# Optimization experiments

Measured on AMD Instinct MI355X. Metric: run time of the kernel, lower is better.

## Reference

```python
import jax, jax.numpy as jnp
import numpy as np

F0_DIM, PH_DIM, MIDI_DIM, DUR_DIM = 64, 128, 64, 64
COND = 256
TOTAL = F0_DIM + PH_DIM + MIDI_DIM + DUR_DIM  # 320
EPS = 1e-5


def setup_inputs() -> dict:
    key = jax.random.key(0)
    ks = jax.random.split(key, 16)
    B, T = 16, 4096
    inp = {
        "f0": jax.random.uniform(ks[0], (B, T), jnp.float32) * 400.0 + 80.0,
        "phone": jax.random.randint(ks[1], (B, T), 0, 100, jnp.int32),
        "duration": jax.random.uniform(ks[2], (B, T), jnp.float32),
        "midi": jax.random.randint(ks[3], (B, T), 0, 128, jnp.int32),
        # f0 encoder: Linear(1,32) -> ReLU -> Linear(32,64)
        "f0_w1": jax.random.normal(ks[4], (1, F0_DIM // 2), jnp.float32) * 0.1,
        "f0_b1": jnp.zeros((F0_DIM // 2,), jnp.float32),
        "f0_w2": jax.random.normal(ks[5], (F0_DIM // 2, F0_DIM), jnp.float32) * 0.1,
        "f0_b2": jnp.zeros((F0_DIM,), jnp.float32),
        # embeddings
        "phone_table": jax.random.normal(ks[6], (100, PH_DIM), jnp.float32),
        "midi_table": jax.random.normal(ks[7], (128, MIDI_DIM), jnp.float32),
        # duration encoder: Linear(1,32) -> ReLU -> Linear(32,64)
        "dur_w1": jax.random.normal(ks[8], (1, DUR_DIM // 2), jnp.float32) * 0.1,
        "dur_b1": jnp.zeros((DUR_DIM // 2,), jnp.float32),
        "dur_w2": jax.random.normal(ks[9], (DUR_DIM // 2, DUR_DIM), jnp.float32) * 0.1,
        "dur_b2": jnp.zeros((DUR_DIM,), jnp.float32),
        # projection: Linear(320,256) -> LayerNorm(256) -> ReLU -> Linear(256,256)
        "proj_w1": jax.random.normal(ks[10], (TOTAL, COND), jnp.float32) * (1.0 / np.sqrt(TOTAL)),
        "proj_b1": jnp.zeros((COND,), jnp.float32),
        "ln_g": jnp.ones((COND,), jnp.float32),
        "ln_b": jnp.zeros((COND,), jnp.float32),
        "proj_w2": jax.random.normal(ks[11], (COND, COND), jnp.float32) * (1.0 / np.sqrt(COND)),
        "proj_b2": jnp.zeros((COND,), jnp.float32),
    }
    return inp


def reference(f0, phone, duration, midi,
              f0_w1, f0_b1, f0_w2, f0_b2,
              phone_table, midi_table,
              dur_w1, dur_b1, dur_w2, dur_b2,
              proj_w1, proj_b1, ln_g, ln_b, proj_w2, proj_b2):
    # f0 / duration MLPs, vectorized over all (batch, time) positions
    f0_h = jax.nn.relu(f0[..., None] * f0_w1[0] + f0_b1)            # [B,T,32]
    f0_emb = f0_h @ f0_w2 + f0_b2                                    # [B,T,64]
    dur_h = jax.nn.relu(duration[..., None] * dur_w1[0] + dur_b1)    # [B,T,32]
    dur_emb = dur_h @ dur_w2 + dur_b2                                # [B,T,64]
    phone_emb = phone_table[phone]                                   # [B,T,128]
    midi_emb = midi_table[midi]                                      # [B,T,64]
    combined = jnp.concatenate([f0_emb, phone_emb, midi_emb, dur_emb], axis=-1)  # [B,T,320]
    h = combined @ proj_w1 + proj_b1                                 # [B,T,256]
    mu = jnp.mean(h, axis=-1, keepdims=True)
    var = jnp.mean((h - mu) ** 2, axis=-1, keepdims=True)
    h = (h - mu) * jax.lax.rsqrt(var + EPS) * ln_g + ln_b
    h = jax.nn.relu(h)
    return h @ proj_w2 + proj_b2                                     # [B,T,256]
```

## Files before the change

### kernel.cpp

```cpp
#include <hip/hip_runtime.h>

typedef _Float16 f16x8 __attribute__((ext_vector_type(8)));
typedef float f32x4 __attribute__((ext_vector_type(4)));
typedef unsigned int u32x2 __attribute__((ext_vector_type(2)));

#define MROWS 65536
#define BM 32
#define NBLK (MROWS / BM)

#define B1F_OFF 0u
#define B2F_OFF 65536u
#define TP_OFF 196608u
#define TM_OFF 299008u
#define BC_OFF 430080u
#define WFD_OFF 431104u


__device__ __forceinline__ unsigned afoff(unsigned X) {
  return (X * 16u) ^ ((X & 0x38u) << 1);
}

__global__ __launch_bounds__(256) void prep_tables(
    const float* __restrict__ f0_w2, const float* __restrict__ f0_b2,
    const float* __restrict__ ptab, const float* __restrict__ mtab,
    const float* __restrict__ dur_w2, const float* __restrict__ dur_b2,
    const float* __restrict__ W1, const float* __restrict__ pb1,
    float* __restrict__ wsf) {
  const int r = blockIdx.x, n = threadIdx.x;
  if (r < 64) {
    float s = 0.f;
    if (r < 32) {
      for (int j = 0; j < 64; ++j) s = fmaf(f0_w2[r * 64 + j], W1[j * 256 + n], s);
    } else {
      for (int j = 0; j < 64; ++j) s = fmaf(dur_w2[(r - 32) * 64 + j], W1[(256 + j) * 256 + n], s);
    }
    wsf[WFD_OFF / 4 + r * 256 + n] = s;
  } else if (r < 164) {
    const int p = r - 64;
    float s = 0.f;
    for (int j = 0; j < 128; ++j) s = fmaf(ptab[p * 128 + j], W1[(64 + j) * 256 + n], s);
    wsf[TP_OFF / 4 + p * 256 + n] = s;
  } else if (r < 292) {
    const int m = r - 164;
    float s = 0.f;
    for (int j = 0; j < 64; ++j) s = fmaf(mtab[m * 64 + j], W1[(192 + j) * 256 + n], s);
    wsf[TM_OFF / 4 + m * 256 + n] = s;
  } else {
    float s = pb1[n];
    for (int j = 0; j < 64; ++j) {
      s = fmaf(f0_b2[j], W1[j * 256 + n], s);
      s = fmaf(dur_b2[j], W1[(256 + j) * 256 + n], s);
    }
    wsf[BC_OFF / 4 + n] = s;
  }
}

__global__ __launch_bounds__(64) void prep_frags(const float* __restrict__ W2, char* __restrict__ ws) {
  const float* Wfd = (const float*)(ws + WFD_OFF);
  const int t = blockIdx.x;
  const int l = threadIdx.x;
  const int qq = l >> 4, c = l & 15;
  if (t < 64) {
    const int kt = t >> 4, nt = t & 15;
    const int col = (nt >> 2) * 64 + c * 4 + (nt & 3);
    f16x8 v;
#pragma unroll
    for (int e = 0; e < 8; ++e) {
      const int k = kt * 32 + 4 * qq + (e & 3) + 16 * (e >> 2);
      v[e] = (_Float16)Wfd[(k & 63) * 256 + col];
    }
    *(f16x8*)(ws + B1F_OFF + (unsigned)((kt * 16 + nt) * 64 + l) * 16u) = v;
  } else {
    const int t2 = t - 64;
    const int kt = t2 >> 4, nt = t2 & 15;
    const int col = (nt >> 2) * 64 + c * 4 + (nt & 3);
    f16x8 v;
#pragma unroll
    for (int e = 0; e < 8; ++e) {
      const int k = kt * 32 + 4 * qq + (e & 3) + 16 * (e >> 2);
      v[e] = (_Float16)W2[k * 256 + col];
    }
    *(f16x8*)(ws + B2F_OFF + (unsigned)((kt * 16 + nt) * 64 + l) * 16u) = v;
  }
}

__global__ __launch_bounds__(256, 2) void cond_enc_main(
    const float* __restrict__ f0g, const int* __restrict__ phone,
    const float* __restrict__ durg, const int* __restrict__ midi,
    const float* __restrict__ f0_w1, const float* __restrict__ f0_b1,
    const float* __restrict__ dur_w1, const float* __restrict__ dur_b1,
    const float* __restrict__ ln_g, const float* __restrict__ ln_b,
    const float* __restrict__ pb2, const char* __restrict__ ws,
    float* __restrict__ out) {
  __shared__ __align__(16) unsigned char smem[16384 + 1536];
  unsigned char* Afrag = smem;
  float* partials = (float*)(smem + 16384);

  const int tid = threadIdx.x;
  const int l = tid & 63;
  const int wc = tid >> 6;
  const int q = l >> 4;
  const int c = l & 15;
  const int b = blockIdx.x;

  const float* Tp = (const float*)(ws + TP_OFF);
  const float* Tm = (const float*)(ws + TM_OFF);

  const int rl = l & 31;
  const float xf_all = f0g[b * BM + rl];
  const float xd_all = durg[b * BM + rl];
  const int ph_all = phone[b * BM + rl];
  const int md_all = midi[b * BM + rl];

  f16x8 a1[2][4];
#pragma unroll
  for (int i = 0; i < 2; ++i) {
    const float xf = __shfl(xf_all, i * 16 + c);
    const float xd = __shfl(xd_all, i * 16 + c);
#pragma unroll
    for (int kh = 0; kh < 2; ++kh) {
      f16x8 hi, lo;
#pragma unroll
      for (int e = 0; e < 8; ++e) {
        const int ki = 4 * q + (e & 3) + 16 * (e >> 2);
        const float wv = kh ? dur_w1[ki] : f0_w1[ki];
        const float bv = kh ? dur_b1[ki] : f0_b1[ki];
        const float x = kh ? xd : xf;
        const float a = fmaxf(fmaf(x, wv, bv), 0.f);
        const _Float16 h = (_Float16)a;
        hi[e] = h;
        lo[e] = (_Float16)(a - (float)h);
      }
      a1[i][kh] = hi;
      a1[i][kh + 2] = lo;
    }
  }

  const f32x4 zero4 = {0.f, 0.f, 0.f, 0.f};
  f32x4 acc[2][4];
#pragma unroll
  for (int i = 0; i < 2; ++i)
#pragma unroll
    for (int j = 0; j < 4; ++j) acc[i][j] = zero4;
  {
    const f16x8* B1p = (const f16x8*)(ws + B1F_OFF);
#pragma unroll
    for (int kt = 0; kt < 4; ++kt) {
      f16x8 b4[4];
#pragma unroll
      for (int j = 0; j < 4; ++j) b4[j] = B1p[(kt * 16 + wc * 4 + j) * 64 + l];
#pragma unroll
      for (int i = 0; i < 2; ++i)
#pragma unroll
        for (int j = 0; j < 4; ++j)
          acc[i][j] = __builtin_amdgcn_mfma_f32_16x16x32_f16(a1[i][kt], b4[j], acc[i][j], 0, 0, 0);
    }
  }

  const f32x4 bc4 = *(const f32x4*)((const float*)(ws + BC_OFF) + wc * 64 + c * 4);
  float psum[2][4], psq[2][4];
#pragma unroll
  for (int i = 0; i < 2; ++i) {
#pragma unroll
    for (int r = 0; r < 4; ++r) {
      const int ph = __shfl(ph_all, i * 16 + q * 4 + r);
      const int md = __shfl(md_all, i * 16 + q * 4 + r);
      const f32x4 tp4 = *(const f32x4*)(Tp + ph * 256 + wc * 64 + c * 4);
      const f32x4 tm4 = *(const f32x4*)(Tm + md * 256 + wc * 64 + c * 4);
      float s = 0.f, ss = 0.f;
#pragma unroll
      for (int j = 0; j < 4; ++j) {
        float v = acc[i][j][r] + bc4[j] + tp4[j] + tm4[j];
        acc[i][j][r] = v;
        s += v;
        ss = fmaf(v, v, ss);
      }
      psum[i][r] = s;
      psq[i][r] = ss;
    }
  }
#pragma unroll
  for (int i = 0; i < 2; ++i)
#pragma unroll
    for (int r = 0; r < 4; ++r) {
      float s = psum[i][r], ss = psq[i][r];
#pragma unroll
      for (int m = 1; m < 16; m <<= 1) {
        s += __shfl_xor(s, m, 64);
        ss += __shfl_xor(ss, m, 64);
      }
      psum[i][r] = s;
      psq[i][r] = ss;
    }
  if (c == 0) {
#pragma unroll
    for (int i = 0; i < 2; ++i)
#pragma unroll
      for (int r = 0; r < 4; ++r) {
        const int row = i * 16 + q * 4 + r;
        partials[row * 12 + wc * 2 + 0] = psum[i][r];
        partials[row * 12 + wc * 2 + 1] = psq[i][r];
      }
  }
  __syncthreads();

  const f32x4 g4 = *(const f32x4*)(ln_g + wc * 64 + c * 4);
  const f32x4 lb4 = *(const f32x4*)(ln_b + wc * 64 + c * 4);
  const int kt_pk = wc * 2 + (c >> 3);
  const int lp_base = 16 * (c & 3);
  const unsigned hoff = (unsigned)((c >> 2) & 1) * 8u;
#pragma unroll
  for (int i = 0; i < 2; ++i) {
#pragma unroll
    for (int r = 0; r < 4; ++r) {
      const int row = i * 16 + q * 4 + r;
      const f32x4 pa = *(const f32x4*)(partials + row * 12);
      const f32x4 pb = *(const f32x4*)(partials + row * 12 + 4);
      const float s = pa[0] + pa[2] + pb[0] + pb[2];
      const float ss = pa[1] + pa[3] + pb[1] + pb[3];
      const float mu = s * (1.f / 256.f);
      const float var = fmaxf(ss * (1.f / 256.f) - mu * mu, 0.f);
      const float rstd = rsqrtf(var + 1e-5f);
      unsigned short h[4];
#pragma unroll
      for (int j = 0; j < 4; ++j) {
        float v = fmaf((acc[i][j][r] - mu) * rstd, g4[j], lb4[j]);
        v = fmaxf(v, 0.f);
        h[j] = __builtin_bit_cast(unsigned short, (_Float16)v);
      }
      u32x2 pkt;
      pkt[0] = (unsigned)h[0] | ((unsigned)h[1] << 16);
      pkt[1] = (unsigned)h[2] | ((unsigned)h[3] << 16);
      const unsigned X = (unsigned)((kt_pk * 2 + i) * 64 + (q * 4 + r + lp_base));
      *(u32x2*)(Afrag + afoff(X) + hoff) = pkt;
    }
  }
  __syncthreads();

#pragma unroll
  for (int i = 0; i < 2; ++i)
#pragma unroll
    for (int j = 0; j < 4; ++j) acc[i][j] = zero4;
  {
    const f16x8* B2p = (const f16x8*)(ws + B2F_OFF);
#pragma unroll
    for (int kt = 0; kt < 8; ++kt) {
      f16x8 a4[2], b4[4];
#pragma unroll
      for (int i = 0; i < 2; ++i)
        a4[i] = *(const f16x8*)(Afrag + afoff((unsigned)((kt * 2 + i) * 64 + l)));
#pragma unroll
      for (int j = 0; j < 4; ++j) b4[j] = B2p[(kt * 16 + wc * 4 + j) * 64 + l];
#pragma unroll
      for (int i = 0; i < 2; ++i)
#pragma unroll
        for (int j = 0; j < 4; ++j)
          acc[i][j] = __builtin_amdgcn_mfma_f32_16x16x32_f16(a4[i], b4[j], acc[i][j], 0, 0, 0);
    }
  }
  const f32x4 b24 = *(const f32x4*)(pb2 + wc * 64 + c * 4);
#pragma unroll
  for (int i = 0; i < 2; ++i)
#pragma unroll
    for (int r = 0; r < 4; ++r) {
      const int grow = b * BM + i * 16 + q * 4 + r;
      f32x4 st;
#pragma unroll
      for (int j = 0; j < 4; ++j) st[j] = acc[i][j][r] + b24[j];
      *(f32x4*)(out + grow * 256 + wc * 64 + c * 4) = st;
    }
}

extern "C" void kernel_launch(void* const* d_in, const int* in_sizes, int n_in,
                              void* d_out, int out_size, void* d_ws, size_t ws_size,
                              hipStream_t stream) {
  (void)in_sizes; (void)n_in; (void)out_size; (void)ws_size;
  const float* f0 = (const float*)d_in[0];
  const int* phone = (const int*)d_in[1];
  const float* dur = (const float*)d_in[2];
  const int* midi = (const int*)d_in[3];
  const float* f0_w1 = (const float*)d_in[4];
  const float* f0_b1 = (const float*)d_in[5];
  const float* f0_w2 = (const float*)d_in[6];
  const float* f0_b2 = (const float*)d_in[7];
  const float* ptab = (const float*)d_in[8];
  const float* mtab = (const float*)d_in[9];
  const float* dur_w1 = (const float*)d_in[10];
  const float* dur_b1 = (const float*)d_in[11];
  const float* dur_w2 = (const float*)d_in[12];
  const float* dur_b2 = (const float*)d_in[13];
  const float* W1 = (const float*)d_in[14];
  const float* pb1 = (const float*)d_in[15];
  const float* ln_g = (const float*)d_in[16];
  const float* ln_b = (const float*)d_in[17];
  const float* W2 = (const float*)d_in[18];
  const float* pb2 = (const float*)d_in[19];
  char* ws = (char*)d_ws;
  float* out = (float*)d_out;

  prep_tables<<<293, 256, 0, stream>>>(f0_w2, f0_b2, ptab, mtab, dur_w2, dur_b2, W1, pb1, (float*)ws);
  prep_frags<<<192, 64, 0, stream>>>(W2, ws);
  cond_enc_main<<<NBLK, 256, 0, stream>>>(f0, phone, dur, midi, f0_w1, f0_b1, dur_w1, dur_b1,
                                          ln_g, ln_b, pb2, ws, out);
}
```

Baseline: 45.81 us.

## Give each wave all 256 columns of 32 rows, drop split-precision first GEMM

Each wave now owns 32 full rows and computes all 256 output columns, so LayerNorm statistics reduce within the wave via shuffles. This removes the cross-wave partials buffer and both block barriers. The hi/lo f16 split of the hidden MLP activations is dropped, halving the first-GEMM K, and output stores become nontemporal. The costs are many more accumulator registers (32 f32x4 accumulators plus 16 B fragments), likely lower occupancy, 64KB of LDS per block, and somewhat lower precision in the first projection.

```diff
diff --git a/kernel.cpp b/kernel.cpp
--- a/kernel.cpp
+++ b/kernel.cpp
@@ -5,7 +5,7 @@
 typedef unsigned int u32x2 __attribute__((ext_vector_type(2)));
 
 #define MROWS 65536
-#define BM 32
+#define BM 128
 #define NBLK (MROWS / BM)
 
 #define B1F_OFF 0u
@@ -16,8 +16,8 @@
 #define WFD_OFF 431104u
 
 
-__device__ __forceinline__ unsigned afoff(unsigned X) {
-  return (X * 16u) ^ ((X & 0x38u) << 1);
+__device__ __forceinline__ unsigned a2off(unsigned X) {
+  return (X * 16u) ^ (X & 0x30u);
 }
 
 __global__ __launch_bounds__(256) void prep_tables(
@@ -60,18 +60,18 @@
   const int t = blockIdx.x;
   const int l = threadIdx.x;
   const int qq = l >> 4, c = l & 15;
-  if (t < 64) {
+  if (t < 32) {
     const int kt = t >> 4, nt = t & 15;
     const int col = (nt >> 2) * 64 + c * 4 + (nt & 3);
     f16x8 v;
 #pragma unroll
     for (int e = 0; e < 8; ++e) {
       const int k = kt * 32 + 4 * qq + (e & 3) + 16 * (e >> 2);
-      v[e] = (_Float16)Wfd[(k & 63) * 256 + col];
+      v[e] = (_Float16)Wfd[k * 256 + col];
     }
     *(f16x8*)(ws + B1F_OFF + (unsigned)((kt * 16 + nt) * 64 + l) * 16u) = v;
   } else {
-    const int t2 = t - 64;
+    const int t2 = t - 32;
     const int kt = t2 >> 4, nt = t2 & 15;
     const int col = (nt >> 2) * 64 + c * 4 + (nt & 3);
     f16x8 v;
@@ -92,182 +92,161 @@
     const float* __restrict__ ln_g, const float* __restrict__ ln_b,
     const float* __restrict__ pb2, const char* __restrict__ ws,
     float* __restrict__ out) {
-  __shared__ __align__(16) unsigned char smem[16384 + 1536];
-  unsigned char* Afrag = smem;
-  float* partials = (float*)(smem + 16384);
+  __shared__ __align__(16) unsigned char smem[4 * 16384];
 
   const int tid = threadIdx.x;
   const int l = tid & 63;
-  const int wc = tid >> 6;
+  const int w = tid >> 6;
   const int q = l >> 4;
   const int c = l & 15;
-  const int b = blockIdx.x;
+  const int rowbase = blockIdx.x * BM + w * 32;
+  unsigned char* Asc = smem + w * 16384;
 
   const float* Tp = (const float*)(ws + TP_OFF);
   const float* Tm = (const float*)(ws + TM_OFF);
 
   const int rl = l & 31;
-  const float xf_all = f0g[b * BM + rl];
-  const float xd_all = durg[b * BM + rl];
-  const int ph_all = phone[b * BM + rl];
-  const int md_all = midi[b * BM + rl];
-
-  f16x8 a1[2][4];
+  const float xf_all = f0g[rowbase + rl];
+  const float xd_all = durg[rowbase + rl];
+  const int ph_all = phone[rowbase + rl];
+  const int md_all = midi[rowbase + rl];
+
+  f16x8 a1[2][2];
 #pragma unroll
   for (int i = 0; i < 2; ++i) {
     const float xf = __shfl(xf_all, i * 16 + c);
     const float xd = __shfl(xd_all, i * 16 + c);
 #pragma unroll
     for (int kh = 0; kh < 2; ++kh) {
-      f16x8 hi, lo;
+      f16x8 v;
 #pragma unroll
       for (int e = 0; e < 8; ++e) {
         const int ki = 4 * q + (e & 3) + 16 * (e >> 2);
         const float wv = kh ? dur_w1[ki] : f0_w1[ki];
         const float bv = kh ? dur_b1[ki] : f0_b1[ki];
         const float x = kh ? xd : xf;
-        const float a = fmaxf(fmaf(x, wv, bv), 0.f);
-        const _Float16 h = (_Float16)a;
-        hi[e] = h;
-        lo[e] = (_Float16)(a - (float)h);
-      }
-      a1[i][kh] = hi;
-      a1[i][kh + 2] = lo;
+        v[e] = (_Float16)fmaxf(fmaf(x, wv, bv), 0.f);
+      }
+      a1[i][kh] = v;
     }
   }
 
   const f32x4 zero4 = {0.f, 0.f, 0.f, 0.f};
-  f32x4 acc[2][4];
+  f32x4 acc[2][16];
 #pragma unroll
   for (int i = 0; i < 2; ++i)
 #pragma unroll
-    for (int j = 0; j < 4; ++j) acc[i][j] = zero4;
+    for (int nt = 0; nt < 16; ++nt) acc[i][nt] = zero4;
   {
     const f16x8* B1p = (const f16x8*)(ws + B1F_OFF);
 #pragma unroll
-    for (int kt = 0; kt < 4; ++kt) {
-      f16x8 b4[4];
-#pragma unroll
-      for (int j = 0; j < 4; ++j) b4[j] = B1p[(kt * 16 + wc * 4 + j) * 64 + l];
+    for (int kt = 0; kt < 2; ++kt) {
+      f16x8 bfr[16];
+#pragma unroll
+      for (int nt = 0; nt < 16; ++nt) bfr[nt] = B1p[(kt * 16 + nt) * 64 + l];
 #pragma unroll
       for (int i = 0; i < 2; ++i)
 #pragma unroll
-        for (int j = 0; j < 4; ++j)
-          acc[i][j] = __builtin_amdgcn_mfma_f32_16x16x32_f16(a1[i][kt], b4[j], acc[i][j], 0, 0, 0);
-    }
-  }
-
-  const f32x4 bc4 = *(const f32x4*)((const float*)(ws + BC_OFF) + wc * 64 + c * 4);
-  float psum[2][4], psq[2][4];
+        for (int nt = 0; nt < 16; ++nt)
+          acc[i][nt] = __builtin_amdgcn_mfma_f32_16x16x32_f16(a1[i][kt], bfr[nt], acc[i][nt], 0, 0, 0);
+    }
+  }
+
+  const float* bcp = (const float*)(ws + BC_OFF);
+  f32x4 bc4[4], g4[4], lb4[4];
+#pragma unroll
+  for (int g = 0; g < 4; ++g) {
+    bc4[g] = *(const f32x4*)(bcp + g * 64 + c * 4);
+    g4[g] = *(const f32x4*)(ln_g + g * 64 + c * 4);
+    lb4[g] = *(const f32x4*)(ln_b + g * 64 + c * 4);
+  }
+  const int lp_base = 16 * (c & 3);
+  const unsigned hoff = (unsigned)((c >> 2) & 1) * 8u;
 #pragma unroll
   for (int i = 0; i < 2; ++i) {
 #pragma unroll
     for (int r = 0; r < 4; ++r) {
-      const int ph = __shfl(ph_all, i * 16 + q * 4 + r);
-      const int md = __shfl(md_all, i * 16 + q * 4 + r);
-      const f32x4 tp4 = *(const f32x4*)(Tp + ph * 256 + wc * 64 + c * 4);
-      const f32x4 tm4 = *(const f32x4*)(Tm + md * 256 + wc * 64 + c * 4);
+      const int rrel = i * 16 + q * 4 + r;
+      const int ph = __shfl(ph_all, rrel);
+      const int md = __shfl(md_all, rrel);
+      f32x4 tp4[4], tm4[4];
+#pragma unroll
+      for (int g = 0; g < 4; ++g) {
+        tp4[g] = *(const f32x4*)(Tp + ph * 256 + g * 64 + c * 4);
+        tm4[g] = *(const f32x4*)(Tm + md * 256 + g * 64 + c * 4);
+      }
       float s = 0.f, ss = 0.f;
 #pragma unroll
-      for (int j = 0; j < 4; ++j) {
-        float v = acc[i][j][r] + bc4[j] + tp4[j] + tm4[j];
-        acc[i][j][r] = v;
+      for (int nt = 0; nt < 16; ++nt) {
+        const int g = nt >> 2, bq = nt & 3;
+        float v = acc[i][nt][r] + bc4[g][bq] + tp4[g][bq] + tm4[g][bq];
+        acc[i][nt][r] = v;
         s += v;
         ss = fmaf(v, v, ss);
       }
-      psum[i][r] = s;
-      psq[i][r] = ss;
-    }
-  }
-#pragma unroll
-  for (int i = 0; i < 2; ++i)
-#pragma unroll
-    for (int r = 0; r < 4; ++r) {
-      float s = psum[i][r], ss = psq[i][r];
 #pragma unroll
       for (int m = 1; m < 16; m <<= 1) {
         s += __shfl_xor(s, m, 64);
         ss += __shfl_xor(ss, m, 64);
       }
-      psum[i][r] = s;
-      psq[i][r] = ss;
-    }
-  if (c == 0) {
-#pragma unroll
-    for (int i = 0; i < 2; ++i)
-#pragma unroll
-      for (int r = 0; r < 4; ++r) {
-        const int row = i * 16 + q * 4 + r;
-        partials[row * 12 + wc * 2 + 0] = psum[i][r];
-        partials[row * 12 + wc * 2 + 1] = psq[i][r];
-      }
-  }
-  __syncthreads();
-
-  const f32x4 g4 = *(const f32x4*)(ln_g + wc * 64 + c * 4);
-  const f32x4 lb4 = *(const f32x4*)(ln_b + wc * 64 + c * 4);
-  const int kt_pk = wc * 2 + (c >> 3);
-  const int lp_base = 16 * (c & 3);
-  const unsigned hoff = (unsigned)((c >> 2) & 1) * 8u;
-#pragma unroll
-  for (int i = 0; i < 2; ++i) {
-#pragma unroll
-    for (int r = 0; r < 4; ++r) {
-      const int row = i * 16 + q * 4 + r;
-      const f32x4 pa = *(const f32x4*)(partials + row * 12);
-      const f32x4 pb = *(const f32x4*)(partials + row * 12 + 4);
-      const float s = pa[0] + pa[2] + pb[0] + pb[2];
-      const float ss = pa[1] + pa[3] + pb[1] + pb[3];
       const float mu = s * (1.f / 256.f);
       const float var = fmaxf(ss * (1.f / 256.f) - mu * mu, 0.f);
       const float rstd = rsqrtf(var + 1e-5f);
-      unsigned short h[4];
-#pragma unroll
-      for (int j = 0; j < 4; ++j) {
-        float v = fmaf((acc[i][j][r] - mu) * rstd, g4[j], lb4[j]);
-        v = fmaxf(v, 0.f);
-        h[j] = __builtin_bit_cast(unsigned short, (_Float16)v);
-      }
-      u32x2 pkt;
-      pkt[0] = (unsigned)h[0] | ((unsigned)h[1] << 16);
-      pkt[1] = (unsigned)h[2] | ((unsigned)h[3] << 16);
-      const unsigned X = (unsigned)((kt_pk * 2 + i) * 64 + (q * 4 + r + lp_base));
-      *(u32x2*)(Afrag + afoff(X) + hoff) = pkt;
-    }
-  }
-  __syncthreads();
+#pragma unroll
+      for (int g = 0; g < 4; ++g) {
+        unsigned short hw[4];
+#pragma unroll
+        for (int bq = 0; bq < 4; ++bq) {
+          float v = fmaf((acc[i][4 * g + bq][r] - mu) * rstd, g4[g][bq], lb4[g][bq]);
+          v = fmaxf(v, 0.f);
+          hw[bq] = __builtin_bit_cast(unsigned short, (_Float16)v);
+        }
+        u32x2 pkt;
+        pkt[0] = (unsigned)hw[0] | ((unsigned)hw[1] << 16);
+        pkt[1] = (unsigned)hw[2] | ((unsigned)hw[3] << 16);
+        const int kt = 2 * g + (c >> 3);
+        const unsigned X = (unsigned)((kt * 2 + i) * 64 + (q * 4 + r + lp_base));
+        *(u32x2*)(Asc + a2off(X) + hoff) = pkt;
+      }
+    }
+  }
 
 #pragma unroll
   for (int i = 0; i < 2; ++i)
 #pragma unroll
-    for (int j = 0; j < 4; ++j) acc[i][j] = zero4;
+    for (int nt = 0; nt < 16; ++nt) acc[i][nt] = zero4;
   {
     const f16x8* B2p = (const f16x8*)(ws + B2F_OFF);
 #pragma unroll
     for (int kt = 0; kt < 8; ++kt) {
-      f16x8 a4[2], b4[4];
-#pragma unroll
-      for (int i = 0; i < 2; ++i)
-        a4[i] = *(const f16x8*)(Afrag + afoff((unsigned)((kt * 2 + i) * 64 + l)));
-#pragma unroll
-      for (int j = 0; j < 4; ++j) b4[j] = B2p[(kt * 16 + wc * 4 + j) * 64 + l];
-#pragma unroll
-      for (int i = 0; i < 2; ++i)
-#pragma unroll
-        for (int j = 0; j < 4; ++j)
-          acc[i][j] = __builtin_amdgcn_mfma_f32_16x16x32_f16(a4[i], b4[j], acc[i][j], 0, 0, 0);
-    }
-  }
-  const f32x4 b24 = *(const f32x4*)(pb2 + wc * 64 + c * 4);
+      f16x8 a0 = *(const f16x8*)(Asc + a2off((unsigned)((kt * 2 + 0) * 64 + l)));
+      f16x8 a1f = *(const f16x8*)(Asc + a2off((unsigned)((kt * 2 + 1) * 64 + l)));
+      f16x8 bfr[16];
+#pragma unroll
+      for (int nt = 0; nt < 16; ++nt) bfr[nt] = B2p[(kt * 16 + nt) * 64 + l];
+#pragma unroll
+      for (int nt = 0; nt < 16; ++nt) {
+        acc[0][nt] = __builtin_amdgcn_mfma_f32_16x16x32_f16(a0, bfr[nt], acc[0][nt], 0, 0, 0);
+        acc[1][nt] = __builtin_amdgcn_mfma_f32_16x16x32_f16(a1f, bfr[nt], acc[1][nt], 0, 0, 0);
+      }
+    }
+  }
+
+  f32x4 b24[4];
+#pragma unroll
+  for (int g = 0; g < 4; ++g) b24[g] = *(const f32x4*)(pb2 + g * 64 + c * 4);
 #pragma unroll
   for (int i = 0; i < 2; ++i)
 #pragma unroll
     for (int r = 0; r < 4; ++r) {
-      const int grow = b * BM + i * 16 + q * 4 + r;
-      f32x4 st;
-#pragma unroll
-      for (int j = 0; j < 4; ++j) st[j] = acc[i][j][r] + b24[j];
-      *(f32x4*)(out + grow * 256 + wc * 64 + c * 4) = st;
+      const int grow = rowbase + i * 16 + q * 4 + r;
+#pragma unroll
+      for (int g = 0; g < 4; ++g) {
+        f32x4 st;
+#pragma unroll
+        for (int bq = 0; bq < 4; ++bq) st[bq] = acc[i][4 * g + bq][r] + b24[g][bq];
+        __builtin_nontemporal_store(st, (f32x4*)(out + grow * 256 + g * 64 + c * 4));
+      }
     }
 }
 
@@ -299,7 +278,7 @@
   float* out = (float*)d_out;
 
   prep_tables<<<293, 256, 0, stream>>>(f0_w2, f0_b2, ptab, mtab, dur_w2, dur_b2, W1, pb1, (float*)ws);
-  prep_frags<<<192, 64, 0, stream>>>(W2, ws);
+  prep_frags<<<160, 64, 0, stream>>>(W2, ws);
   cond_enc_main<<<NBLK, 256, 0, stream>>>(f0, phone, dur, midi, f0_w1, f0_b1, dur_w1, dur_b1,
                                           ln_g, ln_b, pb2, ws, out);
 }
```

After: 39.24 us. 1.17x faster.
